# Performance work log

Hardware: AMD Instinct MI355X
Metric: run time of the kernel (lower is better)

## Reference

```python
import jax, jax.numpy as jnp
import numpy as np

H = 512          # hidden_size
DEPTH = 6        # number of tanh layers
N = 8192         # collocation points
DT = 0.1         # uniform time step
MIN_ALPHA = 0.6  # initial_params['min_alpha']


def _xavier(k, fi, fo):
    lim = np.sqrt(6.0 / (fi + fo))
    return jax.random.uniform(k, (fi, fo), minval=-lim, maxval=lim, dtype=jnp.float32)


def _raw(x):
    # inverse-softplus style init used by EpiPINN: raw = x + log(-expm1(-x))
    return jnp.array([x + np.log(-np.expm1(-x))], dtype=jnp.float32)


def setup_inputs() -> dict:
    key = jax.random.key(0)
    ks = jax.random.split(key, DEPTH + 2)
    W_in = _xavier(ks[0], 1, H)
    b_in = jnp.zeros((H,), jnp.float32)
    Wh = jnp.stack([_xavier(ks[1 + l], H, H) for l in range(DEPTH - 1)])  # [DEPTH-1,H,H]
    bh = jnp.zeros((DEPTH - 1, H), jnp.float32)
    W_out = _xavier(ks[DEPTH], H, 5)
    b_out = jnp.zeros((5,), jnp.float32)
    t = (jnp.arange(N, dtype=jnp.float32) * DT).reshape(N, 1)
    return {
        't': t,
        'W_in': W_in, 'b_in': b_in, 'Wh': Wh, 'bh': bh,
        'W_out': W_out, 'b_out': b_out,
        'raw_beta': _raw(0.3), 'raw_sigma': _raw(0.2),
        'raw_gamma': _raw(0.1), 'raw_mu': _raw(0.05),
        'z_alpha': jnp.array([0.0], dtype=jnp.float32),
    }


def _forward_all(t, W_in, b_in, Wh, bh, W_out, b_out,
                 raw_beta, raw_sigma, raw_gamma, raw_mu, z_alpha):
    # --- PINN MLP: 1 -> H (tanh) x DEPTH -> 5, softmax over components ---
    h = jnp.tanh(t @ W_in + b_in)
    for l in range(Wh.shape[0]):  # static small loop over layers
        h = jnp.tanh(h @ Wh[l] + bh[l])
    y = jax.nn.softmax(h @ W_out + b_out, axis=1)  # [n,5]

    alpha = MIN_ALPHA + (1.0 - MIN_ALPHA) * jax.nn.sigmoid(z_alpha[0])
    beta = jax.nn.softplus(raw_beta[0])
    sigma = jax.nn.softplus(raw_sigma[0])
    gamma = jax.nn.softplus(raw_gamma[0])
    mu = jax.nn.softplus(raw_mu[0])

    # --- Caputo L1 fractional derivative for all 5 components at once ---
    n = y.shape[0]
    dpsi = y[1:] - y[:-1]  # [n-1,5] first differences
    rs = jnp.arange(n - 1, dtype=y.dtype)
    rs_safe = jnp.where(rs == 0, 1.0, rs)  # avoid 0**x grad nan; value unchanged
    ws = (rs + 1.0) ** (1.0 - alpha) - jnp.where(rs == 0, 0.0, rs_safe ** (1.0 - alpha))
    C = DT ** (-alpha) / jnp.exp(jax.lax.lgamma(2.0 - alpha))
    ii = jnp.arange(n - 1)
    idx = ii[:, None] - ii[None, :]
    A = jnp.where(idx >= 0, ws[jnp.clip(idx, 0)], 0.0)  # lower-triangular Toeplitz [n-1,n-1]
    dfrac = jnp.concatenate([jnp.zeros((1, 5), y.dtype), C * (A @ dpsi)], axis=0)  # [n,5]

    # --- SEIRD right-hand side and physics residual ---
    s, e, i, r, d = (y[:, k:k + 1] for k in range(5))
    living = 1.0 - d
    inf_term = beta * s * i / living
    f = jnp.concatenate([
        -inf_term,
        inf_term - sigma * e,
        sigma * e - (gamma + mu) * i,
        gamma * i,
        mu * i,
    ], axis=1)  # [n,5]
    return jnp.mean((dfrac - f) ** 2)


def reference(t, W_in, b_in, Wh, bh, W_out, b_out,
              raw_beta, raw_sigma, raw_gamma, raw_mu, z_alpha):
    return _forward_all(t, W_in, b_in, Wh, bh, W_out, b_out,
                        raw_beta, raw_sigma, raw_gamma, raw_mu, z_alpha)
```

## Files before the change

kernel.cpp:

```cpp
#include <hip/hip_runtime.h>
#include <math.h>

typedef short short8v __attribute__((ext_vector_type(8)));
typedef float float4v __attribute__((ext_vector_type(4)));

#define N_PTS 8192
#define HDIM  512
#define NHID  5
#define KSTR  1024

#define OFF_XA    0ull
#define OFF_XB    16777216ull
#define OFF_WT    33554432ull
#define OFF_Y     38797312ull
#define OFF_DPSI  38961152ull
#define OFF_WSW   39124992ull
#define OFF_PART  39157760ull
#define OFF_BPART 40468480ull

__device__ __forceinline__ unsigned short f2bf(float x) {
  unsigned u = __builtin_bit_cast(unsigned, x);
  u += 0x7FFFu + ((u >> 16) & 1u);
  return (unsigned short)(u >> 16);
}
__device__ __forceinline__ float bf2f(unsigned short h) {
  unsigned u = ((unsigned)h) << 16;
  return __builtin_bit_cast(float, u);
}

#define GLOAD16(gsrc, ldst) \
  __builtin_amdgcn_global_load_lds( \
      (const __attribute__((address_space(1))) void*)(gsrc), \
      (__attribute__((address_space(3))) void*)(ldst), 16, 0, 0)

__global__ void wprep_kernel(const float* __restrict__ Wh,
                             unsigned short* __restrict__ WT) {
  __shared__ float tile[32][33];
  int l = blockIdx.z;
  int kb = blockIdx.x;
  int n0 = blockIdx.y * 32;
  int j = threadIdx.x & 31, i8 = threadIdx.x >> 5;
  const float* W = Wh + (size_t)l * HDIM * HDIM;
#pragma unroll
  for (int q = 0; q < 4; ++q)
    tile[i8 + 8 * q][j] = W[(size_t)(kb * 32 + i8 + 8 * q) * HDIM + n0 + j];
  __syncthreads();
#pragma unroll
  for (int q = 0; q < 4; ++q) {
    int n = n0 + i8 + 8 * q;
    float v = tile[j][i8 + 8 * q];
    unsigned short h = f2bf(v);
    unsigned short lo = f2bf(v - bf2f(h));
    size_t o = ((size_t)l * HDIM + n) * KSTR + kb * 64 + j;
    WT[o] = h; WT[o + 32] = lo;
  }
}

__global__ void layer0_kernel(const float* __restrict__ t,
                              const float* __restrict__ Win,
                              const float* __restrict__ bin,
                              unsigned short* __restrict__ X) {
  int gid = blockIdx.x * blockDim.x + threadIdx.x;
  int row = gid >> 7;
  int jq  = (gid & 127) << 2;
  float tv = t[row];
  float4 w = *(const float4*)(Win + jq);
  float4 b = *(const float4*)(bin + jq);
  float v[4];
  v[0] = tanhf(tv * w.x + b.x); v[1] = tanhf(tv * w.y + b.y);
  v[2] = tanhf(tv * w.z + b.z); v[3] = tanhf(tv * w.w + b.w);
  ushort4 h4, l4;
  h4.x = f2bf(v[0]); l4.x = f2bf(v[0] - bf2f(h4.x));
  h4.y = f2bf(v[1]); l4.y = f2bf(v[1] - bf2f(h4.y));
  h4.z = f2bf(v[2]); l4.z = f2bf(v[2] - bf2f(h4.z));
  h4.w = f2bf(v[3]); l4.w = f2bf(v[3] - bf2f(h4.w));
  size_t o = (size_t)row * KSTR + (jq >> 5) * 64 + (jq & 31);
  *(ushort4*)(X + o) = h4;
  *(ushort4*)(X + o + 32) = l4;
}

__global__ __launch_bounds__(256) void gemm_split_kernel(
    const unsigned short* __restrict__ A,
    const unsigned short* __restrict__ Bt,
    const float* __restrict__ bias,
    unsigned short* __restrict__ C) {
  __shared__ __align__(16) short lds[2][12288];
  const int tid = threadIdx.x;
  const int lane = tid & 63, w = tid >> 6;
  const int wr = w >> 1, wc = w & 1;
  const int r0 = blockIdx.x * 128, c0 = blockIdx.y * 64;
  const int rl = lane & 15, kgrp = lane >> 4;

  float4v acc[4][2];
#pragma unroll
  for (int i = 0; i < 4; ++i)
#pragma unroll
    for (int j = 0; j < 2; ++j) acc[i][j] = (float4v){0.f, 0.f, 0.f, 0.f};

  auto stage = [&](int b, int kt) {
    const int kbase = kt * 64;
#pragma unroll
    for (int i = 0; i < 4; ++i) {
      int c = i * 256 + tid;
      int row = c >> 3, m = c & 7;
      int gs = m ^ (row & 7);
      GLOAD16(A + (size_t)(r0 + row) * KSTR + kbase + gs * 8,
              &lds[b][(i * 256 + w * 64) * 8]);
    }
#pragma unroll
    for (int i = 0; i < 2; ++i) {
      int c = i * 256 + tid;
      int col = c >> 3, m = c & 7;
      int gs = m ^ (col & 7);
      GLOAD16(Bt + (size_t)(c0 + col) * KSTR + kbase + gs * 8,
              &lds[b][8192 + (i * 256 + w * 64) * 8]);
    }
  };

  stage(0, 0);
  __syncthreads();
  int cur = 0;

#pragma unroll 1
  for (int kt = 0; kt < 16; ++kt) {
    if (kt < 15) stage(cur ^ 1, kt + 1);
    const short* bufc = lds[cur];
    short8v ahi[4], alo[4], bhi[2], blo[2];
#pragma unroll
    for (int mi = 0; mi < 4; ++mi) {
      int row = wr * 64 + mi * 16 + rl;
      int sh = kgrp ^ (row & 7);
      int sl = (kgrp + 4) ^ (row & 7);
      ahi[mi] = *(const short8v*)&bufc[row * 64 + sh * 8];
      alo[mi] = *(const short8v*)&bufc[row * 64 + sl * 8];
    }
#pragma unroll
    for (int ni = 0; ni < 2; ++ni) {
      int col = wc * 32 + ni * 16 + rl;
      int sh = kgrp ^ (col & 7);
      int sl = (kgrp + 4) ^ (col & 7);
      bhi[ni] = *(const short8v*)&bufc[8192 + col * 64 + sh * 8];
      blo[ni] = *(const short8v*)&bufc[8192 + col * 64 + sl * 8];
    }
#pragma unroll
    for (int mi = 0; mi < 4; ++mi)
#pragma unroll
      for (int ni = 0; ni < 2; ++ni)
        acc[mi][ni] = __builtin_amdgcn_mfma_f32_16x16x32_bf16(ahi[mi], bhi[ni], acc[mi][ni], 0, 0, 0);
#pragma unroll
    for (int mi = 0; mi < 4; ++mi)
#pragma unroll
      for (int ni = 0; ni < 2; ++ni)
        acc[mi][ni] = __builtin_amdgcn_mfma_f32_16x16x32_bf16(ahi[mi], blo[ni], acc[mi][ni], 0, 0, 0);
#pragma unroll
    for (int mi = 0; mi < 4; ++mi)
#pragma unroll
      for (int ni = 0; ni < 2; ++ni)
        acc[mi][ni] = __builtin_amdgcn_mfma_f32_16x16x32_bf16(alo[mi], bhi[ni], acc[mi][ni], 0, 0, 0);
    __syncthreads();
    cur ^= 1;
  }

  float bcol[2];
#pragma unroll
  for (int ni = 0; ni < 2; ++ni) bcol[ni] = bias[c0 + wc * 32 + ni * 16 + rl];
#pragma unroll
  for (int mi = 0; mi < 4; ++mi)
#pragma unroll
    for (int ni = 0; ni < 2; ++ni)
#pragma unroll
      for (int r = 0; r < 4; ++r) {
        int row = r0 + wr * 64 + mi * 16 + kgrp * 4 + r;
        int col = c0 + wc * 32 + ni * 16 + rl;
        float v = tanhf(acc[mi][ni][r] + bcol[ni]);
        unsigned short h = f2bf(v);
        unsigned short lo = f2bf(v - bf2f(h));
        size_t o = (size_t)row * KSTR + (col >> 5) * 64 + (col & 31);
        C[o] = h; C[o + 32] = lo;
      }
}

__global__ void outlayer_kernel(const unsigned short* __restrict__ X,
                                const float* __restrict__ Wout,
                                const float* __restrict__ bout,
                                float* __restrict__ y) {
  int wid  = threadIdx.x >> 6;
  int lane = threadIdx.x & 63;
  int row  = blockIdx.x * 4 + wid;
  float acc[5] = {0.f, 0.f, 0.f, 0.f, 0.f};
  for (int k = lane; k < HDIM; k += 64) {
    size_t o = (size_t)row * KSTR + (k >> 5) * 64 + (k & 31);
    float hv = bf2f(X[o]) + bf2f(X[o + 32]);
    const float* wr = Wout + k * 5;
#pragma unroll
    for (int c = 0; c < 5; ++c) acc[c] += hv * wr[c];
  }
#pragma unroll
  for (int c = 0; c < 5; ++c)
    for (int off = 32; off; off >>= 1) acc[c] += __shfl_down(acc[c], off);
  if (lane == 0) {
    float l[5], m = -1e30f;
#pragma unroll
    for (int c = 0; c < 5; ++c) { l[c] = acc[c] + bout[c]; m = fmaxf(m, l[c]); }
    float s = 0.f;
#pragma unroll
    for (int c = 0; c < 5; ++c) { l[c] = expf(l[c] - m); s += l[c]; }
    float inv = 1.f / s;
#pragma unroll
    for (int c = 0; c < 5; ++c) y[row * 5 + c] = l[c] * inv;
  }
}

__global__ void wsw_kernel(const float* __restrict__ z_alpha,
                           float* __restrict__ wsw) {
  int r = blockIdx.x * blockDim.x + threadIdx.x;
  if (r >= N_PTS - 1) return;
  double z = (double)z_alpha[0];
  double alpha = 0.6 + 0.4 / (1.0 + exp(-z));
  double p = 1.0 - alpha;
  double w = pow((double)r + 1.0, p) - (r == 0 ? 0.0 : pow((double)r, p));
  wsw[r] = (float)w;
}

__global__ void dpsi_kernel(const float* __restrict__ y, float* __restrict__ dpsi) {
  int g = blockIdx.x * blockDim.x + threadIdx.x;
  if (g < (N_PTS - 1) * 5) dpsi[g] = y[g + 5] - y[g];
}

#define CHUNK 1024
#define JT 256
__global__ __launch_bounds__(256) void conv_kernel(
    const float* __restrict__ dpsi, const float* __restrict__ wsw,
    float* __restrict__ part) {
  __shared__ float dps[JT * 5];
  __shared__ float wsl[512];
  int tid = threadIdx.x;
  int r0  = blockIdx.x * 256;
  int ch  = blockIdx.y;
  int r   = r0 + tid;
  float acc[5] = {0.f, 0.f, 0.f, 0.f, 0.f};

  for (int t4 = 0; t4 < CHUNK / JT; ++t4) {
    int j0 = ch * CHUNK + t4 * JT;
    if (j0 > r0 + 254) break;
#pragma unroll
    for (int s = 0; s < 5; ++s) dps[tid + s * 256] = dpsi[j0 * 5 + tid + s * 256];
    int base = r0 - j0 - 256;
#pragma unroll
    for (int s = 0; s < 2; ++s) {
      int i = tid + s * 256;
      int src = base + i;
      wsl[i] = (src >= 0 && src < N_PTS - 1) ? wsw[src] : 0.f;
    }
    __syncthreads();
    int widx = tid + 255;
    if (j0 + JT <= r) {
#pragma unroll 4
      for (int jj = 0; jj < JT; ++jj) {
        float w = wsl[widx - jj];
        const float* dp = &dps[jj * 5];
        acc[0] += w * dp[0]; acc[1] += w * dp[1]; acc[2] += w * dp[2];
        acc[3] += w * dp[3]; acc[4] += w * dp[4];
      }
    } else {
      int nj = r - j0;
      if (nj > JT) nj = JT;
      for (int jj = 0; jj < nj; ++jj) {
        float w = wsl[widx - jj];
        const float* dp = &dps[jj * 5];
        acc[0] += w * dp[0]; acc[1] += w * dp[1]; acc[2] += w * dp[2];
        acc[3] += w * dp[3]; acc[4] += w * dp[4];
      }
    }
    __syncthreads();
  }
  float* p = part + ((size_t)ch * N_PTS + r) * 5;
  p[0] = acc[0]; p[1] = acc[1]; p[2] = acc[2]; p[3] = acc[3]; p[4] = acc[4];
}

__device__ __forceinline__ float softplusf_(float x) {
  return x > 20.f ? x : log1pf(expf(x));
}

__global__ void combine_kernel(const float* __restrict__ y,
                               const float* __restrict__ part,
                               const float* __restrict__ rb, const float* __restrict__ rs,
                               const float* __restrict__ rg, const float* __restrict__ rm,
                               const float* __restrict__ za,
                               float* __restrict__ bpart) {
  __shared__ float red[256];
  int tid = threadIdx.x;
  int row = blockIdx.x * 256 + tid;

  float beta  = softplusf_(rb[0]);
  float sigma = softplusf_(rs[0]);
  float gamma = softplusf_(rg[0]);
  float mu    = softplusf_(rm[0]);
  double z = (double)za[0];
  double alpha = 0.6 + 0.4 / (1.0 + exp(-z));
  float C = (float)(pow(0.1, -alpha) / tgamma(2.0 - alpha));

  float df[5];
  if (row == 0) {
    df[0] = df[1] = df[2] = df[3] = df[4] = 0.f;
  } else {
#pragma unroll
    for (int c = 0; c < 5; ++c) {
      float s = 0.f;
#pragma unroll
      for (int ch = 0; ch < 8; ++ch)
        s += part[((size_t)ch * N_PTS + row) * 5 + c];
      df[c] = C * s;
    }
  }
  float yv[5];
#pragma unroll
  for (int c = 0; c < 5; ++c) yv[c] = y[row * 5 + c];
  float living = 1.f - yv[4];
  float inf_t = beta * yv[0] * yv[2] / living;
  float f[5];
  f[0] = -inf_t;
  f[1] = inf_t - sigma * yv[1];
  f[2] = sigma * yv[1] - (gamma + mu) * yv[2];
  f[3] = gamma * yv[2];
  f[4] = mu * yv[2];
  float s = 0.f;
#pragma unroll
  for (int c = 0; c < 5; ++c) { float d = df[c] - f[c]; s += d * d; }

  red[tid] = s;
  __syncthreads();
  for (int off = 128; off; off >>= 1) {
    if (tid < off) red[tid] += red[tid + off];
    __syncthreads();
  }
  if (tid == 0) bpart[blockIdx.x] = red[0];
}

__global__ void finish_kernel(const float* __restrict__ bpart, float* __restrict__ out) {
  if (threadIdx.x == 0) {
    float s = 0.f;
    for (int i = 0; i < 32; ++i) s += bpart[i];
    out[0] = s / (float)(N_PTS * 5);
  }
}

extern "C" void kernel_launch(void* const* d_in, const int* in_sizes, int n_in,
                              void* d_out, int out_size, void* d_ws, size_t ws_size,
                              hipStream_t stream) {
  const float* t     = (const float*)d_in[0];
  const float* W_in  = (const float*)d_in[1];
  const float* b_in  = (const float*)d_in[2];
  const float* Wh    = (const float*)d_in[3];
  const float* bh    = (const float*)d_in[4];
  const float* W_out = (const float*)d_in[5];
  const float* b_out = (const float*)d_in[6];
  const float* rbta  = (const float*)d_in[7];
  const float* rsig  = (const float*)d_in[8];
  const float* rgam  = (const float*)d_in[9];
  const float* rmu   = (const float*)d_in[10];
  const float* zalp  = (const float*)d_in[11];

  char* wsb = (char*)d_ws;
  unsigned short* XA = (unsigned short*)(wsb + OFF_XA);
  unsigned short* XB = (unsigned short*)(wsb + OFF_XB);
  unsigned short* WT = (unsigned short*)(wsb + OFF_WT);
  float* y     = (float*)(wsb + OFF_Y);
  float* dpsi  = (float*)(wsb + OFF_DPSI);
  float* wsw   = (float*)(wsb + OFF_WSW);
  float* part  = (float*)(wsb + OFF_PART);
  float* bpart = (float*)(wsb + OFF_BPART);
  float* out   = (float*)d_out;

  wprep_kernel<<<dim3(16, 16, 5), 256, 0, stream>>>(Wh, WT);

  layer0_kernel<<<N_PTS * 128 / 256, 256, 0, stream>>>(t, W_in, b_in, XA);

  for (int l = 0; l < NHID; ++l) {
    const unsigned short* in = (l & 1) ? XB : XA;
    unsigned short*      oub = (l & 1) ? XA : XB;
    gemm_split_kernel<<<dim3(N_PTS / 128, HDIM / 64), 256, 0, stream>>>(
        in, WT + (size_t)l * HDIM * KSTR, bh + (size_t)l * HDIM, oub);
  }

  outlayer_kernel<<<N_PTS / 4, 256, 0, stream>>>(XB, W_out, b_out, y);

  wsw_kernel<<<(N_PTS + 255) / 256, 256, 0, stream>>>(zalp, wsw);
  dpsi_kernel<<<((N_PTS - 1) * 5 + 255) / 256, 256, 0, stream>>>(y, dpsi);

  conv_kernel<<<dim3(N_PTS / 256, 8), 256, 0, stream>>>(dpsi, wsw, part);

  combine_kernel<<<N_PTS / 256, 256, 0, stream>>>(y, part, rbta, rsig, rgam, rmu,
                                                  zalp, bpart);
  finish_kernel<<<1, 64, 0, stream>>>(bpart, out);
  (void)in_sizes; (void)n_in; (void)out_size; (void)ws_size;
}
```

Before: 160.4 us.

## Triple-buffer GEMM loads, vectorize output layer, fuse Caputo prep, widen conv split

The hidden-layer GEMM moves from double to triple-buffered LDS staging with explicit vmcnt waits and raw barriers, so global loads run two tiles ahead. The output layer reads 8 bf16 hi/lo pairs per lane as vectors instead of scalar strided loads. The weight and difference prep kernels are merged into one launch. The convolution now splits over 16 chunks of 512 with padded LDS rows read as float4, and its triangular boundary branch is dropped. LDS use per GEMM block grows and combine reads twice as many partials. The conv chunk with the diagonal now relies on zero-padded weights for correctness.

```diff
diff --git a/kernel.cpp b/kernel.cpp
--- a/kernel.cpp
+++ b/kernel.cpp
@@ -8,6 +8,7 @@
 #define HDIM  512
 #define NHID  5
 #define KSTR  1024
+#define NCH   16
 
 #define OFF_XA    0ull
 #define OFF_XB    16777216ull
@@ -16,7 +17,7 @@
 #define OFF_DPSI  38961152ull
 #define OFF_WSW   39124992ull
 #define OFF_PART  39157760ull
-#define OFF_BPART 40468480ull
+#define OFF_BPART 41779200ull
 
 __device__ __forceinline__ unsigned short f2bf(float x) {
   unsigned u = __builtin_bit_cast(unsigned, x);
@@ -84,7 +85,7 @@
     const unsigned short* __restrict__ Bt,
     const float* __restrict__ bias,
     unsigned short* __restrict__ C) {
-  __shared__ __align__(16) short lds[2][12288];
+  __shared__ __align__(16) short lds[3][12288];
   const int tid = threadIdx.x;
   const int lane = tid & 63, w = tid >> 6;
   const int wr = w >> 1, wc = w & 1;
@@ -118,13 +119,15 @@
   };
 
   stage(0, 0);
-  __syncthreads();
-  int cur = 0;
+  stage(1, 1);
+  asm volatile("s_waitcnt vmcnt(6)" ::: "memory");
+  __builtin_amdgcn_s_barrier();
+  asm volatile("" ::: "memory");
 
 #pragma unroll 1
   for (int kt = 0; kt < 16; ++kt) {
-    if (kt < 15) stage(cur ^ 1, kt + 1);
-    const short* bufc = lds[cur];
+    if (kt < 14) stage((kt + 2) % 3, kt + 2);
+    const short* bufc = lds[kt % 3];
     short8v ahi[4], alo[4], bhi[2], blo[2];
 #pragma unroll
     for (int mi = 0; mi < 4; ++mi) {
@@ -157,8 +160,12 @@
 #pragma unroll
       for (int ni = 0; ni < 2; ++ni)
         acc[mi][ni] = __builtin_amdgcn_mfma_f32_16x16x32_bf16(alo[mi], bhi[ni], acc[mi][ni], 0, 0, 0);
-    __syncthreads();
-    cur ^= 1;
+    if (kt < 15) {
+      if (kt < 14) asm volatile("s_waitcnt vmcnt(6)" ::: "memory");
+      else         asm volatile("s_waitcnt vmcnt(0)" ::: "memory");
+      __builtin_amdgcn_s_barrier();
+      asm volatile("" ::: "memory");
+    }
   }
 
   float bcol[2];
@@ -187,13 +194,16 @@
   int wid  = threadIdx.x >> 6;
   int lane = threadIdx.x & 63;
   int row  = blockIdx.x * 4 + wid;
+  size_t o = (size_t)row * KSTR + (lane >> 2) * 64 + (lane & 3) * 8;
+  short8v hv = *(const short8v*)(X + o);
+  short8v lv = *(const short8v*)(X + o + 32);
+  const float* wrp = Wout + lane * 40;
   float acc[5] = {0.f, 0.f, 0.f, 0.f, 0.f};
-  for (int k = lane; k < HDIM; k += 64) {
-    size_t o = (size_t)row * KSTR + (k >> 5) * 64 + (k & 31);
-    float hv = bf2f(X[o]) + bf2f(X[o + 32]);
-    const float* wr = Wout + k * 5;
-#pragma unroll
-    for (int c = 0; c < 5; ++c) acc[c] += hv * wr[c];
+#pragma unroll
+  for (int e = 0; e < 8; ++e) {
+    float h = bf2f((unsigned short)hv[e]) + bf2f((unsigned short)lv[e]);
+#pragma unroll
+    for (int c = 0; c < 5; ++c) acc[c] += h * wrp[e * 5 + c];
   }
 #pragma unroll
   for (int c = 0; c < 5; ++c)
@@ -211,28 +221,25 @@
   }
 }
 
-__global__ void wsw_kernel(const float* __restrict__ z_alpha,
-                           float* __restrict__ wsw) {
-  int r = blockIdx.x * blockDim.x + threadIdx.x;
-  if (r >= N_PTS - 1) return;
-  double z = (double)z_alpha[0];
-  double alpha = 0.6 + 0.4 / (1.0 + exp(-z));
-  double p = 1.0 - alpha;
-  double w = pow((double)r + 1.0, p) - (r == 0 ? 0.0 : pow((double)r, p));
-  wsw[r] = (float)w;
-}
-
-__global__ void dpsi_kernel(const float* __restrict__ y, float* __restrict__ dpsi) {
+__global__ void prep_caputo_kernel(const float* __restrict__ z_alpha,
+                                   const float* __restrict__ y,
+                                   float* __restrict__ wsw,
+                                   float* __restrict__ dpsi) {
   int g = blockIdx.x * blockDim.x + threadIdx.x;
   if (g < (N_PTS - 1) * 5) dpsi[g] = y[g + 5] - y[g];
-}
-
-#define CHUNK 1024
-#define JT 256
+  if (g < N_PTS - 1) {
+    double z = (double)z_alpha[0];
+    double alpha = 0.6 + 0.4 / (1.0 + exp(-z));
+    double p = 1.0 - alpha;
+    double w = pow((double)g + 1.0, p) - (g == 0 ? 0.0 : pow((double)g, p));
+    wsw[g] = (float)w;
+  }
+}
+
 __global__ __launch_bounds__(256) void conv_kernel(
     const float* __restrict__ dpsi, const float* __restrict__ wsw,
     float* __restrict__ part) {
-  __shared__ float dps[JT * 5];
+  __shared__ float dps[256][8];
   __shared__ float wsl[512];
   int tid = threadIdx.x;
   int r0  = blockIdx.x * 256;
@@ -240,11 +247,15 @@
   int r   = r0 + tid;
   float acc[5] = {0.f, 0.f, 0.f, 0.f, 0.f};
 
-  for (int t4 = 0; t4 < CHUNK / JT; ++t4) {
-    int j0 = ch * CHUNK + t4 * JT;
+  for (int t4 = 0; t4 < 2; ++t4) {
+    int j0 = ch * 512 + t4 * 256;
     if (j0 > r0 + 254) break;
-#pragma unroll
-    for (int s = 0; s < 5; ++s) dps[tid + s * 256] = dpsi[j0 * 5 + tid + s * 256];
+    __syncthreads();
+    {
+      const float* dr = dpsi + (size_t)(j0 + tid) * 5;
+      dps[tid][0] = dr[0]; dps[tid][1] = dr[1]; dps[tid][2] = dr[2];
+      dps[tid][3] = dr[3]; dps[tid][4] = dr[4];
+    }
     int base = r0 - j0 - 256;
 #pragma unroll
     for (int s = 0; s < 2; ++s) {
@@ -254,25 +265,14 @@
     }
     __syncthreads();
     int widx = tid + 255;
-    if (j0 + JT <= r) {
 #pragma unroll 4
-      for (int jj = 0; jj < JT; ++jj) {
-        float w = wsl[widx - jj];
-        const float* dp = &dps[jj * 5];
-        acc[0] += w * dp[0]; acc[1] += w * dp[1]; acc[2] += w * dp[2];
-        acc[3] += w * dp[3]; acc[4] += w * dp[4];
-      }
-    } else {
-      int nj = r - j0;
-      if (nj > JT) nj = JT;
-      for (int jj = 0; jj < nj; ++jj) {
-        float w = wsl[widx - jj];
-        const float* dp = &dps[jj * 5];
-        acc[0] += w * dp[0]; acc[1] += w * dp[1]; acc[2] += w * dp[2];
-        acc[3] += w * dp[3]; acc[4] += w * dp[4];
-      }
-    }
-    __syncthreads();
+    for (int jj = 0; jj < 256; ++jj) {
+      float w = wsl[widx - jj];
+      float4 d4 = *(const float4*)&dps[jj][0];
+      float d5 = dps[jj][4];
+      acc[0] += w * d4.x; acc[1] += w * d4.y; acc[2] += w * d4.z;
+      acc[3] += w * d4.w; acc[4] += w * d5;
+    }
   }
   float* p = part + ((size_t)ch * N_PTS + r) * 5;
   p[0] = acc[0]; p[1] = acc[1]; p[2] = acc[2]; p[3] = acc[3]; p[4] = acc[4];
@@ -308,7 +308,7 @@
     for (int c = 0; c < 5; ++c) {
       float s = 0.f;
 #pragma unroll
-      for (int ch = 0; ch < 8; ++ch)
+      for (int ch = 0; ch < NCH; ++ch)
         s += part[((size_t)ch * N_PTS + row) * 5 + c];
       df[c] = C * s;
     }
@@ -385,10 +385,9 @@
 
   outlayer_kernel<<<N_PTS / 4, 256, 0, stream>>>(XB, W_out, b_out, y);
 
-  wsw_kernel<<<(N_PTS + 255) / 256, 256, 0, stream>>>(zalp, wsw);
-  dpsi_kernel<<<((N_PTS - 1) * 5 + 255) / 256, 256, 0, stream>>>(y, dpsi);
-
-  conv_kernel<<<dim3(N_PTS / 256, 8), 256, 0, stream>>>(dpsi, wsw, part);
+  prep_caputo_kernel<<<160, 256, 0, stream>>>(zalp, y, wsw, dpsi);
+
+  conv_kernel<<<dim3(N_PTS / 256, NCH), 256, 0, stream>>>(dpsi, wsw, part);
 
   combine_kernel<<<N_PTS / 256, 256, 0, stream>>>(y, part, rbta, rsig, rgam, rmu,
                                                   zalp, bpart);
```

Result: faster. 143.3 us (-10.7%).
